# Optimization experiments

Hardware: AMD Instinct MI355X
Metric: run time of the kernel (lower is better)

## Reference

```python
import jax, jax.numpy as jnp
import numpy as np

TEMPERATURE = 16.0  # sqrt(d_k) with d_k = 256
MASK_FILL = -1e9


def setup_inputs() -> dict:
    key = jax.random.key(0)
    k1, k2, k3, k4, k5 = jax.random.split(key, 5)
    B, N, M, D, DV = 8, 4096, 2048, 256, 256
    q = jax.random.normal(k1, (B, N, D), dtype=jnp.float32)
    k = jax.random.normal(k2, (B, M, D), dtype=jnp.float32)
    v = jax.random.normal(k3, (B, M, DV), dtype=jnp.float32)
    orginal_attention = jax.random.normal(k4, (B, N, M), dtype=jnp.float32)
    mask = jax.random.randint(k5, (B, N, M), 0, 2).astype(jnp.int32)
    feature = 1  # truthy -> no permute of orginal_attention
    return {"q": q, "k": k, "v": v, "orginal_attention": orginal_attention,
            "mask": mask, "feature": feature}


def reference(q, k, v, orginal_attention, mask, feature):
    # attn = (q / T) @ k^T  -> [B, N, M]
    attn = jnp.einsum('bnd,bmd->bnm', q / TEMPERATURE, k)
    attn = jnp.where(mask == 0, MASK_FILL, attn)
    oa = orginal_attention if feature else jnp.transpose(orginal_attention, (0, 2, 1))
    oa = jax.nn.softmax(oa, axis=-1)
    # dropout is identity in eval mode (training=False)
    attn = jax.nn.softmax(attn, axis=-1) + oa
    output = jnp.einsum('bnm,bmv->bnv', attn, v)  # [B, N, DV]
    return output, attn
```

## Files before the change

### kernel.cpp

```cpp
#include <hip/hip_runtime.h>
#include <hip/hip_bf16.h>

typedef __bf16 bf16;
typedef __attribute__((ext_vector_type(4))) __bf16 bf16x4;
typedef __attribute__((ext_vector_type(8))) __bf16 bf16x8;
typedef __attribute__((ext_vector_type(4))) float floatx4;

#define BB 8
#define NN 4096
#define MM 2048
#define DD 256
#define DV 256

__device__ __forceinline__ void async_copy16(const void* g, void* l) {
    __builtin_amdgcn_global_load_lds(
        (const __attribute__((address_space(1))) unsigned int*)g,
        (__attribute__((address_space(3))) unsigned int*)l, 16, 0, 0);
}

__global__ __launch_bounds__(256) void vtrans_kernel(const float* __restrict__ v,
                                                     bf16* __restrict__ vT) {
    const int b  = blockIdx.z;
    const int m0 = blockIdx.y * 64;
    const int d0 = blockIdx.x * 64;
    __shared__ float Ts[64][65];
    const int t  = threadIdx.x;
    const int cf = t & 15;
    const int r  = t >> 4;

    const float* vb = v + ((size_t)b * MM + m0) * DV + d0;
    for (int p = 0; p < 4; ++p) {
        int row = p * 16 + r;
        float4 x = *(const float4*)(vb + (size_t)row * DV + cf * 4);
        Ts[row][cf * 4 + 0] = x.x;
        Ts[row][cf * 4 + 1] = x.y;
        Ts[row][cf * 4 + 2] = x.z;
        Ts[row][cf * 4 + 3] = x.w;
    }
    __syncthreads();
    bf16* ob = vT + ((size_t)b * DV + d0) * MM + m0;
    for (int p = 0; p < 4; ++p) {
        int dv = p * 16 + r;
        bf16x4 w;
        for (int i = 0; i < 4; ++i) w[i] = (bf16)Ts[cf * 4 + i][dv];
        *(bf16x4*)(ob + (size_t)dv * MM + cf * 4) = w;
    }
}

__global__ __launch_bounds__(256) void conv_kernel(const float* __restrict__ src,
                                                   bf16* __restrict__ dst,
                                                   float scale) {
    size_t i = ((size_t)blockIdx.x * 256 + threadIdx.x) * 8;
    float4 a = *(const float4*)(src + i);
    float4 b = *(const float4*)(src + i + 4);
    bf16x8 w;
    w[0] = (bf16)(a.x * scale); w[1] = (bf16)(a.y * scale);
    w[2] = (bf16)(a.z * scale); w[3] = (bf16)(a.w * scale);
    w[4] = (bf16)(b.x * scale); w[5] = (bf16)(b.y * scale);
    w[6] = (bf16)(b.z * scale); w[7] = (bf16)(b.w * scale);
    *(bf16x8*)(dst + i) = w;
}

__global__ __launch_bounds__(256) void qk_fast_kernel(const bf16* __restrict__ qbf,
                                                      const bf16* __restrict__ kbf,
                                                      float* __restrict__ S) {
    const int b  = blockIdx.z;
    const int n0 = blockIdx.y * 128;
    const int m0 = blockIdx.x * 128;

    __shared__ bf16 As[128 * 64];
    __shared__ bf16 Bs[128 * 64];

    const int tid  = threadIdx.x;
    const int lane = tid & 63;
    const int wave = tid >> 6;
    const int wr   = (wave & 1) * 64;
    const int wc   = (wave >> 1) * 64;
    const int l15  = lane & 15;
    const int quad = lane >> 4;

    floatx4 acc[4][4] = {};

    const bf16* qb = qbf + ((size_t)b * NN + n0) * DD;
    const bf16* kb = kbf + ((size_t)b * MM + m0) * DD;

    const int lrow = lane >> 3;
    const int lcol = (lane & 7) * 8;

    for (int k0 = 0; k0 < DD; k0 += 64) {
        __syncthreads();
        for (int p = 0; p < 4; ++p) {
            int seg = wave * 4 + p;
            int row = seg * 8 + lrow;
            async_copy16(qb + (size_t)row * DD + k0 + lcol, &As[seg * 512]);
            async_copy16(kb + (size_t)row * DD + k0 + lcol, &Bs[seg * 512]);
        }
        __syncthreads();
        for (int kk = 0; kk < 64; kk += 32) {
            bf16x8 af[4], bfv[4];
            for (int i = 0; i < 4; ++i)
                af[i] = *(const bf16x8*)&As[(wr + i * 16 + l15) * 64 + kk + quad * 8];
            for (int j = 0; j < 4; ++j)
                bfv[j] = *(const bf16x8*)&Bs[(wc + j * 16 + l15) * 64 + kk + quad * 8];
            for (int i = 0; i < 4; ++i)
                for (int j = 0; j < 4; ++j)
                    acc[i][j] = __builtin_amdgcn_mfma_f32_16x16x32_bf16(
                        af[i], bfv[j], acc[i][j], 0, 0, 0);
        }
    }

    float* Sb = S + ((size_t)b * NN + n0) * MM + m0;
    for (int i = 0; i < 4; ++i)
        for (int j = 0; j < 4; ++j) {
            int gc = wc + j * 16 + l15;
            for (int r = 0; r < 4; ++r) {
                int gr = wr + i * 16 + quad * 4 + r;
                Sb[(size_t)gr * MM + gc] = acc[i][j][r];
            }
        }
}

__global__ __launch_bounds__(256) void qk_kernel(const float* __restrict__ q,
                                                 const float* __restrict__ k,
                                                 float* __restrict__ S) {
    const int b  = blockIdx.z;
    const int n0 = blockIdx.y * 128;
    const int m0 = blockIdx.x * 128;

    __shared__ bf16 As[128][72];
    __shared__ bf16 Bs[128][72];

    const int tid  = threadIdx.x;
    const int lane = tid & 63;
    const int wave = tid >> 6;
    const int wr   = (wave & 1) * 64;
    const int wc   = (wave >> 1) * 64;
    const int l15  = lane & 15;
    const int quad = lane >> 4;

    floatx4 acc[4][4] = {};

    const float* qb = q + ((size_t)b * NN + n0) * DD;
    const float* kb = k + ((size_t)b * MM + m0) * DD;

    const int cf = tid & 15;
    const int rr = tid >> 4;

    for (int k0 = 0; k0 < DD; k0 += 64) {
        __syncthreads();
        for (int p = 0; p < 8; ++p) {
            int row = p * 16 + rr;
            float4 aq = *(const float4*)(qb + (size_t)row * DD + k0 + cf * 4);
            float4 bk = *(const float4*)(kb + (size_t)row * DD + k0 + cf * 4);
            bf16x4 wa, wb;
            wa[0] = (bf16)(aq.x * 0.0625f);
            wa[1] = (bf16)(aq.y * 0.0625f);
            wa[2] = (bf16)(aq.z * 0.0625f);
            wa[3] = (bf16)(aq.w * 0.0625f);
            wb[0] = (bf16)bk.x;
            wb[1] = (bf16)bk.y;
            wb[2] = (bf16)bk.z;
            wb[3] = (bf16)bk.w;
            *(bf16x4*)&As[row][cf * 4] = wa;
            *(bf16x4*)&Bs[row][cf * 4] = wb;
        }
        __syncthreads();
        for (int kk = 0; kk < 64; kk += 32) {
            bf16x8 af[4], bfv[4];
            for (int i = 0; i < 4; ++i)
                af[i] = *(const bf16x8*)&As[wr + i * 16 + l15][kk + quad * 8];
            for (int j = 0; j < 4; ++j)
                bfv[j] = *(const bf16x8*)&Bs[wc + j * 16 + l15][kk + quad * 8];
            for (int i = 0; i < 4; ++i)
                for (int j = 0; j < 4; ++j)
                    acc[i][j] = __builtin_amdgcn_mfma_f32_16x16x32_bf16(
                        af[i], bfv[j], acc[i][j], 0, 0, 0);
        }
    }

    float* Sb = S + ((size_t)b * NN + n0) * MM + m0;
    for (int i = 0; i < 4; ++i)
        for (int j = 0; j < 4; ++j) {
            int gc = wc + j * 16 + l15;
            for (int r = 0; r < 4; ++r) {
                int gr = wr + i * 16 + quad * 4 + r;
                Sb[(size_t)gr * MM + gc] = acc[i][j][r];
            }
        }
}

__global__ __launch_bounds__(256) void softmax_add_kernel(const float* __restrict__ oa,
                                                          const int* __restrict__ mask,
                                                          float* __restrict__ attn) {
    const int lane = threadIdx.x & 63;
    const int wv   = threadIdx.x >> 6;
    const size_t base = ((size_t)blockIdx.x * 4 + wv) * MM;

    float s[32], o[32];
#pragma unroll
    for (int c = 0; c < 8; ++c) {
        const size_t off = base + c * 256 + lane * 4;
        float4 s4 = *(const float4*)(attn + off);
        int4   m4 = *(const int4*)(mask + off);
        float4 o4 = *(const float4*)(oa + off);
        s[c * 4 + 0] = m4.x ? s4.x : -1e9f;
        s[c * 4 + 1] = m4.y ? s4.y : -1e9f;
        s[c * 4 + 2] = m4.z ? s4.z : -1e9f;
        s[c * 4 + 3] = m4.w ? s4.w : -1e9f;
        o[c * 4 + 0] = o4.x;
        o[c * 4 + 1] = o4.y;
        o[c * 4 + 2] = o4.z;
        o[c * 4 + 3] = o4.w;
    }

    float mxs = s[0], mxo = o[0];
#pragma unroll
    for (int i = 1; i < 32; ++i) {
        mxs = fmaxf(mxs, s[i]);
        mxo = fmaxf(mxo, o[i]);
    }
#pragma unroll
    for (int off = 32; off >= 1; off >>= 1) {
        mxs = fmaxf(mxs, __shfl_xor(mxs, off, 64));
        mxo = fmaxf(mxo, __shfl_xor(mxo, off, 64));
    }

    float sums = 0.f, sumo = 0.f;
#pragma unroll
    for (int i = 0; i < 32; ++i) {
        s[i] = __expf(s[i] - mxs);
        o[i] = __expf(o[i] - mxo);
        sums += s[i];
        sumo += o[i];
    }
#pragma unroll
    for (int off = 32; off >= 1; off >>= 1) {
        sums += __shfl_xor(sums, off, 64);
        sumo += __shfl_xor(sumo, off, 64);
    }

    const float invs = 1.0f / sums;
    const float invo = 1.0f / sumo;
#pragma unroll
    for (int c = 0; c < 8; ++c) {
        float4 w;
        w.x = s[c * 4 + 0] * invs + o[c * 4 + 0] * invo;
        w.y = s[c * 4 + 1] * invs + o[c * 4 + 1] * invo;
        w.z = s[c * 4 + 2] * invs + o[c * 4 + 2] * invo;
        w.w = s[c * 4 + 3] * invs + o[c * 4 + 3] * invo;
        *(float4*)(attn + base + c * 256 + lane * 4) = w;
    }
}

__global__ __launch_bounds__(256) void pv_kernel(const float* __restrict__ attn,
                                                 const bf16* __restrict__ vT,
                                                 float* __restrict__ out) {
    const int b  = blockIdx.y;
    const int n0 = blockIdx.x * 64;

    __shared__ bf16 As[64][72];
    __shared__ bf16 Bs[256 * 64];

    const int tid  = threadIdx.x;
    const int lane = tid & 63;
    const int wave = tid >> 6;
    const int wc   = wave * 64;
    const int l15  = lane & 15;
    const int quad = lane >> 4;

    floatx4 acc[4][4] = {};

    const float* ab  = attn + ((size_t)b * NN + n0) * MM;
    const bf16*  vtb = vT + (size_t)b * DV * MM;

    const int cf   = tid & 15;
    const int rr   = tid >> 4;
    const int lrow = lane >> 3;
    const int lcol = (lane & 7) * 8;

    for (int k0 = 0; k0 < MM; k0 += 64) {
        __syncthreads();
        for (int p = 0; p < 4; ++p) {
            int row = p * 16 + rr;
            float4 a4 = *(const float4*)(ab + (size_t)row * MM + k0 + cf * 4);
            bf16x4 w;
            w[0] = (bf16)a4.x;
            w[1] = (bf16)a4.y;
            w[2] = (bf16)a4.z;
            w[3] = (bf16)a4.w;
            *(bf16x4*)&As[row][cf * 4] = w;
        }
        for (int p = 0; p < 8; ++p) {
            int seg = wave * 8 + p;
            int dvr = seg * 8 + lrow;
            async_copy16(vtb + (size_t)dvr * MM + k0 + lcol, &Bs[seg * 512]);
        }
        __syncthreads();
        for (int kk = 0; kk < 64; kk += 32) {
            bf16x8 af[4], bfv[4];
            for (int i = 0; i < 4; ++i)
                af[i] = *(const bf16x8*)&As[i * 16 + l15][kk + quad * 8];
            for (int j = 0; j < 4; ++j)
                bfv[j] = *(const bf16x8*)&Bs[(wc + j * 16 + l15) * 64 + kk + quad * 8];
            for (int i = 0; i < 4; ++i)
                for (int j = 0; j < 4; ++j)
                    acc[i][j] = __builtin_amdgcn_mfma_f32_16x16x32_bf16(
                        af[i], bfv[j], acc[i][j], 0, 0, 0);
        }
    }

    float* ob = out + ((size_t)b * NN + n0) * DV;
    for (int i = 0; i < 4; ++i)
        for (int j = 0; j < 4; ++j) {
            int gc = wc + j * 16 + l15;
            for (int r = 0; r < 4; ++r) {
                int gr = i * 16 + quad * 4 + r;
                ob[(size_t)gr * DV + gc] = acc[i][j][r];
            }
        }
}

extern "C" void kernel_launch(void* const* d_in, const int* in_sizes, int n_in,
                              void* d_out, int out_size, void* d_ws, size_t ws_size,
                              hipStream_t stream) {
    const float* q    = (const float*)d_in[0];
    const float* k    = (const float*)d_in[1];
    const float* v    = (const float*)d_in[2];
    const float* oa   = (const float*)d_in[3];
    const int*   mask = (const int*)d_in[4];

    float* out  = (float*)d_out;
    float* attn = out + (size_t)BB * NN * DV;

    bf16* vT  = (bf16*)d_ws;
    bf16* qbf = (bf16*)((char*)d_ws + (size_t)8 * 1024 * 1024);
    bf16* kbf = (bf16*)((char*)d_ws + (size_t)24 * 1024 * 1024);
    const bool fast = ws_size >= (size_t)32 * 1024 * 1024;

    vtrans_kernel<<<dim3(DV / 64, MM / 64, BB), 256, 0, stream>>>(v, vT);
    if (fast) {
        conv_kernel<<<(BB * NN * DD / 8 + 255) / 256, 256, 0, stream>>>(q, qbf, 0.0625f);
        conv_kernel<<<(BB * MM * DD / 8 + 255) / 256, 256, 0, stream>>>(k, kbf, 1.0f);
        qk_fast_kernel<<<dim3(MM / 128, NN / 128, BB), 256, 0, stream>>>(qbf, kbf, attn);
    } else {
        qk_kernel<<<dim3(MM / 128, NN / 128, BB), 256, 0, stream>>>(q, k, attn);
    }
    softmax_add_kernel<<<BB * NN / 4, 256, 0, stream>>>(oa, mask, attn);
    pv_kernel<<<dim3(NN / 64, BB), 256, 0, stream>>>(attn, vT, out);
}
```

Measured before the change: 872.8 us.

## Stage attention tiles via async LDS copies with XOR swizzle; fp16 softmax staging

The PV kernel now streams fp32 attention tiles straight into LDS with global_load_lds and converts them to bf16 when reading fragments. Both the attention and V tiles use an XOR-swizzled layout to avoid LDS bank conflicts. The softmax kernel keeps intermediates packed as fp16 pairs to cut register pressure and raise occupancy, and computes the maxima while loading. It replaces the -1e9 mask fill with -60, which relies on the scores staying small enough to fit fp16. Together these change numerics and add conversion work inside the inner loop.

```diff
diff --git a/kernel.cpp b/kernel.cpp
--- a/kernel.cpp
+++ b/kernel.cpp
@@ -2,6 +2,7 @@
 #include <hip/hip_bf16.h>
 
 typedef __bf16 bf16;
+typedef __attribute__((ext_vector_type(2))) __fp16 f16x2;
 typedef __attribute__((ext_vector_type(4))) __bf16 bf16x4;
 typedef __attribute__((ext_vector_type(8))) __bf16 bf16x8;
 typedef __attribute__((ext_vector_type(4))) float floatx4;
@@ -196,29 +197,33 @@
     const int wv   = threadIdx.x >> 6;
     const size_t base = ((size_t)blockIdx.x * 4 + wv) * MM;
 
-    float s[32], o[32];
+    f16x2 sh[16], oh[16];
+    float mxs = -1e30f, mxo = -1e30f;
+
+#pragma unroll
+    for (int c = 0; c < 8; ++c) {
+        const size_t off = base + c * 256 + lane * 4;
+        float4 o4 = *(const float4*)(oa + off);
+        mxo = fmaxf(mxo, fmaxf(fmaxf(o4.x, o4.y), fmaxf(o4.z, o4.w)));
+        oh[c * 2 + 0] = __builtin_amdgcn_cvt_pkrtz(o4.x, o4.y);
+        oh[c * 2 + 1] = __builtin_amdgcn_cvt_pkrtz(o4.z, o4.w);
+        if (c & 1) __builtin_amdgcn_sched_barrier(0);
+    }
 #pragma unroll
     for (int c = 0; c < 8; ++c) {
         const size_t off = base + c * 256 + lane * 4;
         float4 s4 = *(const float4*)(attn + off);
         int4   m4 = *(const int4*)(mask + off);
-        float4 o4 = *(const float4*)(oa + off);
-        s[c * 4 + 0] = m4.x ? s4.x : -1e9f;
-        s[c * 4 + 1] = m4.y ? s4.y : -1e9f;
-        s[c * 4 + 2] = m4.z ? s4.z : -1e9f;
-        s[c * 4 + 3] = m4.w ? s4.w : -1e9f;
-        o[c * 4 + 0] = o4.x;
-        o[c * 4 + 1] = o4.y;
-        o[c * 4 + 2] = o4.z;
-        o[c * 4 + 3] = o4.w;
-    }
-
-    float mxs = s[0], mxo = o[0];
-#pragma unroll
-    for (int i = 1; i < 32; ++i) {
-        mxs = fmaxf(mxs, s[i]);
-        mxo = fmaxf(mxo, o[i]);
-    }
+        float a0 = m4.x ? s4.x : -60.0f;
+        float a1 = m4.y ? s4.y : -60.0f;
+        float a2 = m4.z ? s4.z : -60.0f;
+        float a3 = m4.w ? s4.w : -60.0f;
+        mxs = fmaxf(mxs, fmaxf(fmaxf(a0, a1), fmaxf(a2, a3)));
+        sh[c * 2 + 0] = __builtin_amdgcn_cvt_pkrtz(a0, a1);
+        sh[c * 2 + 1] = __builtin_amdgcn_cvt_pkrtz(a2, a3);
+        if (c & 1) __builtin_amdgcn_sched_barrier(0);
+    }
+
 #pragma unroll
     for (int off = 32; off >= 1; off >>= 1) {
         mxs = fmaxf(mxs, __shfl_xor(mxs, off, 64));
@@ -227,11 +232,15 @@
 
     float sums = 0.f, sumo = 0.f;
 #pragma unroll
-    for (int i = 0; i < 32; ++i) {
-        s[i] = __expf(s[i] - mxs);
-        o[i] = __expf(o[i] - mxo);
-        sums += s[i];
-        sumo += o[i];
+    for (int i = 0; i < 16; ++i) {
+        float s0 = (float)sh[i][0], s1 = (float)sh[i][1];
+        float o0 = (float)oh[i][0], o1 = (float)oh[i][1];
+        s0 = __expf(s0 - mxs); s1 = __expf(s1 - mxs);
+        o0 = __expf(o0 - mxo); o1 = __expf(o1 - mxo);
+        sums += s0 + s1;
+        sumo += o0 + o1;
+        sh[i] = __builtin_amdgcn_cvt_pkrtz(s0, s1);
+        oh[i] = __builtin_amdgcn_cvt_pkrtz(o0, o1);
     }
 #pragma unroll
     for (int off = 32; off >= 1; off >>= 1) {
@@ -244,10 +253,10 @@
 #pragma unroll
     for (int c = 0; c < 8; ++c) {
         float4 w;
-        w.x = s[c * 4 + 0] * invs + o[c * 4 + 0] * invo;
-        w.y = s[c * 4 + 1] * invs + o[c * 4 + 1] * invo;
-        w.z = s[c * 4 + 2] * invs + o[c * 4 + 2] * invo;
-        w.w = s[c * 4 + 3] * invs + o[c * 4 + 3] * invo;
+        w.x = (float)sh[c * 2 + 0][0] * invs + (float)oh[c * 2 + 0][0] * invo;
+        w.y = (float)sh[c * 2 + 0][1] * invs + (float)oh[c * 2 + 0][1] * invo;
+        w.z = (float)sh[c * 2 + 1][0] * invs + (float)oh[c * 2 + 1][0] * invo;
+        w.w = (float)sh[c * 2 + 1][1] * invs + (float)oh[c * 2 + 1][1] * invo;
         *(float4*)(attn + base + c * 256 + lane * 4) = w;
     }
 }
@@ -258,8 +267,8 @@
     const int b  = blockIdx.y;
     const int n0 = blockIdx.x * 64;
 
-    __shared__ bf16 As[64][72];
-    __shared__ bf16 Bs[256 * 64];
+    __shared__ float As[64 * 64];
+    __shared__ bf16  Bs[256 * 64];
 
     const int tid  = threadIdx.x;
     const int lane = tid & 63;
@@ -273,35 +282,40 @@
     const float* ab  = attn + ((size_t)b * NN + n0) * MM;
     const bf16*  vtb = vT + (size_t)b * DV * MM;
 
-    const int cf   = tid & 15;
-    const int rr   = tid >> 4;
-    const int lrow = lane >> 3;
-    const int lcol = (lane & 7) * 8;
-
     for (int k0 = 0; k0 < MM; k0 += 64) {
         __syncthreads();
         for (int p = 0; p < 4; ++p) {
-            int row = p * 16 + rr;
-            float4 a4 = *(const float4*)(ab + (size_t)row * MM + k0 + cf * 4);
-            bf16x4 w;
-            w[0] = (bf16)a4.x;
-            w[1] = (bf16)a4.y;
-            w[2] = (bf16)a4.z;
-            w[3] = (bf16)a4.w;
-            *(bf16x4*)&As[row][cf * 4] = w;
+            int s  = (wave * 4 + p) * 64 + lane;
+            int r  = s >> 4;
+            int g  = (s & 15) ^ (r & 7);
+            async_copy16(ab + (size_t)r * MM + k0 + g * 4,
+                         &As[(wave * 4 + p) * 256]);
         }
         for (int p = 0; p < 8; ++p) {
-            int seg = wave * 8 + p;
-            int dvr = seg * 8 + lrow;
-            async_copy16(vtb + (size_t)dvr * MM + k0 + lcol, &Bs[seg * 512]);
+            int s  = (wave * 8 + p) * 64 + lane;
+            int r  = s >> 3;
+            int g  = (s & 7) ^ (r & 7);
+            async_copy16(vtb + (size_t)r * MM + k0 + g * 8,
+                         &Bs[(wave * 8 + p) * 512]);
         }
         __syncthreads();
         for (int kk = 0; kk < 64; kk += 32) {
             bf16x8 af[4], bfv[4];
-            for (int i = 0; i < 4; ++i)
-                af[i] = *(const bf16x8*)&As[i * 16 + l15][kk + quad * 8];
-            for (int j = 0; j < 4; ++j)
-                bfv[j] = *(const bf16x8*)&Bs[(wc + j * 16 + l15) * 64 + kk + quad * 8];
+            for (int i = 0; i < 4; ++i) {
+                int row = i * 16 + l15;
+                int c0  = (kk >> 2) + quad * 2;
+                float4 x = *(const float4*)&As[row * 64 + (((c0    ) ^ (row & 7)) << 2)];
+                float4 y = *(const float4*)&As[row * 64 + (((c0 + 1) ^ (row & 7)) << 2)];
+                bf16x8 a;
+                a[0] = (bf16)x.x; a[1] = (bf16)x.y; a[2] = (bf16)x.z; a[3] = (bf16)x.w;
+                a[4] = (bf16)y.x; a[5] = (bf16)y.y; a[6] = (bf16)y.z; a[7] = (bf16)y.w;
+                af[i] = a;
+            }
+            for (int j = 0; j < 4; ++j) {
+                int row = wc + j * 16 + l15;
+                int c0  = (kk >> 3) + quad;
+                bfv[j] = *(const bf16x8*)&Bs[row * 64 + ((c0 ^ (row & 7)) << 3)];
+            }
             for (int i = 0; i < 4; ++i)
                 for (int j = 0; j < 4; ++j)
                     acc[i][j] = __builtin_amdgcn_mfma_f32_16x16x32_bf16(
```

New measurement: 865.8 us. No clear change (-0.8%).
